# Optimization experiments

Measured on AMD Instinct MI355X. Metric: run time of the kernel, lower is better.

The kernel has to match this reference:

```python
import jax, jax.numpy as jnp
import numpy as np

NUM_EDGE_TYPES = 4
TIME_STEPS = (1, 1)  # one propagation step per layer, 2 layers
HIDDEN = 128
N_NODES = 50000
N_EDGES = 400000


def setup_inputs() -> dict:
    key = jax.random.key(0)
    ks = jax.random.split(key, 8)
    states = jax.random.normal(ks[0], (N_NODES, HIDDEN), jnp.float32)
    etype = jax.random.randint(ks[1], (N_EDGES,), 0, NUM_EDGE_TYPES, jnp.int32)
    src = jax.random.randint(ks[2], (N_EDGES,), 0, N_NODES, jnp.int32)
    dst = jax.random.randint(ks[3], (N_EDGES,), 0, N_NODES, jnp.int32)
    edges = jnp.stack([etype, src, dst], axis=-1)  # [E, 3] = (type, src, dst)
    L = len(TIME_STEPS)
    std = HIDDEN ** -0.5  # matches tf.random_normal_initializer(stddev=H**-0.5)
    type_W = jax.random.normal(ks[4], (L, NUM_EDGE_TYPES, HIDDEN, HIDDEN), jnp.float32) * std
    type_b = jax.random.normal(ks[5], (L, NUM_EDGE_TYPES, HIDDEN), jnp.float32) * std
    gru_kernel = jax.random.normal(ks[6], (L, HIDDEN, 3 * HIDDEN), jnp.float32) * std
    gru_rkernel = jax.random.normal(ks[7], (L, HIDDEN, 3 * HIDDEN), jnp.float32) * std
    gru_bias = jnp.zeros((L, 2, 3 * HIDDEN), jnp.float32)  # [input_bias, recurrent_bias]
    return dict(states=states, edges=edges, type_W=type_W, type_b=type_b,
                gru_kernel=gru_kernel, gru_rkernel=gru_rkernel, gru_bias=gru_bias)


def _gru_cell(x, h, kernel, rkernel, bias):
    # tf.keras.layers.GRUCell with defaults (reset_after=True, sigmoid/tanh)
    mx = x @ kernel + bias[0]   # [N, 3H]
    mh = h @ rkernel + bias[1]  # [N, 3H]
    xz, xr, xh = jnp.split(mx, 3, axis=-1)
    hz, hr, hh = jnp.split(mh, 3, axis=-1)
    z = jax.nn.sigmoid(xz + hz)
    r = jax.nn.sigmoid(xr + hr)
    c = jnp.tanh(xh + r * hh)
    return z * h + (1.0 - z) * c


def _propagate(h, layer_no, edges, type_W, type_b):
    etype, src, dst = edges[:, 0], edges[:, 1], edges[:, 2]
    src_states = h[src]  # [E, H] irregular gather
    msgs = jnp.zeros_like(src_states)
    # per-edge-type dense transform, combined via masking (jit-friendly
    # equivalent of tf.dynamic_partition + per-type matmul)
    for t in range(NUM_EDGE_TYPES):
        mt = src_states @ type_W[layer_no, t] + type_b[layer_no, t]
        msgs = msgs + jnp.where((etype == t)[:, None], mt, 0.0)
    # scatter-add messages into destination nodes
    return jax.ops.segment_sum(msgs, dst, num_segments=h.shape[0])


def reference(states, edges, type_W, type_b, gru_kernel, gru_rkernel, gru_bias):
    h = states
    for layer_no, steps in enumerate(TIME_STEPS):
        for _ in range(steps):
            agg = _propagate(h, layer_no, edges, type_W, type_b)
            h = _gru_cell(agg, h, gru_kernel[layer_no], gru_rkernel[layer_no], gru_bias[layer_no])
    return h
```

## Files before the change

### kernel.cpp

```cpp
#include <hip/hip_runtime.h>
#include <hip/hip_bf16.h>

#define H 128
#define NT 4
#define CAP4 40

typedef __attribute__((ext_vector_type(8))) _Float16 half8;
typedef __attribute__((ext_vector_type(8))) unsigned short ushort8;
typedef __attribute__((ext_vector_type(4))) float f32x4;

#if defined(__has_builtin)
#if __has_builtin(__builtin_amdgcn_global_load_lds)
#define HAS_GLL 1
#endif
#endif
#ifndef HAS_GLL
#define HAS_GLL 0
#endif

__device__ __forceinline__ float bf2f(unsigned short u) {
    union { unsigned int i; float f; } v;
    v.i = ((unsigned int)u) << 16;
    return v.f;
}

__device__ __forceinline__ unsigned short f2bf(float f) {
    union { float f; unsigned int i; } v;
    v.f = f;
    unsigned int x = v.i;
    unsigned int r = (x + 0x7fffu + ((x >> 16) & 1u)) >> 16;
    return (unsigned short)r;
}

__device__ __forceinline__ float fsigmoid(float x) {
    return 1.0f / (1.0f + __expf(-x));
}
__device__ __forceinline__ float ftanh(float x) {
    return 1.0f - 2.0f / (__expf(2.0f * x) + 1.0f);
}

__device__ __forceinline__ float readf(const void* p, long i, int isbf) {
    return isbf ? bf2f(((const unsigned short*)p)[i]) : ((const float*)p)[i];
}

__device__ __forceinline__ void gll16(const _Float16* g, _Float16* l) {
#if HAS_GLL
    __builtin_amdgcn_global_load_lds(
        (const __attribute__((address_space(1))) unsigned int*)g,
        (__attribute__((address_space(3))) unsigned int*)l, 16, 0, 0);
#else
    const int lane = threadIdx.x & 63;
    *(half8*)&l[lane * 8] = *(const half8*)g;
#endif
}

__device__ __forceinline__ half8 frag(const _Float16* lds, int r, int g) {
    return *(const half8*)&lds[r * 64 + ((g ^ (r & 7)) * 8)];
}

__global__ void detect_dtype(const unsigned short* __restrict__ states_u16,
                             int* __restrict__ flag) {
    __shared__ int cnt;
    if (threadIdx.x == 0) cnt = 0;
    __syncthreads();
    int local = 0;
    for (int i = threadIdx.x; i < 1024; i += 256) {
        unsigned short u = states_u16[2 * i];
        int e = (u >> 7) & 0xFF;
        if (e >= 96 && e <= 158) local++;
    }
    atomicAdd(&cnt, local);
    __syncthreads();
    if (threadIdx.x == 0) *flag = (cnt >= 512) ? 1 : 0;
}

__global__ void prep_all(
    const void* __restrict__ states, const void* __restrict__ type_W,
    const void* __restrict__ type_b, const void* __restrict__ gk,
    const void* __restrict__ gr, const void* __restrict__ grub,
    _Float16* __restrict__ h16, _Float16* __restrict__ BTw,
    _Float16* __restrict__ BTg, float* __restrict__ btab,
    float* __restrict__ gbsum, float* __restrict__ gb0c,
    float* __restrict__ gb1c, int* __restrict__ counts4,
    const int* __restrict__ flag,
    long NNH, int nBTw, int nBTg, int NC4, int LAYERS) {
    long i = (long)blockIdx.x * 256 + threadIdx.x;
    const int fl = *flag;
    if (i < NNH) {
        h16[i] = (_Float16)readf(states, i, fl);
        return;
    }
    i -= NNH;
    if (i < nBTw) {
        int l = (int)(i >> 16);
        int r16 = (int)(i & 65535);
        int cblk = r16 >> 13;
        int rem = r16 & 8191;
        int g = rem >> 7;
        int mm = (rem >> 3) & 15;
        int j = rem & 7;
        int c = cblk * 16 + mm;
        int k = g * 8 + j;
        int t = k >> 7, kk = k & 127;
        BTw[i] = (_Float16)readf(type_W, (((long)(l * NT + t) * H) + kk) * H + c, fl);
        return;
    }
    i -= nBTw;
    if (i < nBTg) {
        int l = (int)(i >> 17);
        int r17 = (int)(i & 131071);
        int ncblk = r17 >> 12;
        int rem = r17 & 4095;
        int g = rem >> 7;
        int mm = (rem >> 3) & 15;
        int j = rem & 7;
        int nc = ncblk * 16 + mm;
        int k = g * 8 + j;
        int gblk = nc >> 6, gate = (nc >> 4) & 3;
        int c = gblk * 16 + (nc & 15);
        float v = 0.0f;
        if (gate == 0) {
            v = (k < 128) ? readf(gk, ((long)l * H + k) * 384 + c, fl)
                          : readf(gr, ((long)l * H + (k - 128)) * 384 + c, fl);
        } else if (gate == 1) {
            v = (k < 128) ? readf(gk, ((long)l * H + k) * 384 + 128 + c, fl)
                          : readf(gr, ((long)l * H + (k - 128)) * 384 + 128 + c, fl);
        } else if (gate == 2) {
            if (k < 128) v = readf(gk, ((long)l * H + k) * 384 + 256 + c, fl);
        } else {
            if (k >= 128) v = readf(gr, ((long)l * H + (k - 128)) * 384 + 256 + c, fl);
        }
        BTg[i] = (_Float16)v;
        return;
    }
    i -= nBTg;
    if (i < NC4) {
        counts4[i] = 0;
        return;
    }
    i -= NC4;
    {
        int j = (int)i;
        if (j < LAYERS * NT * H) btab[j] = readf(type_b, j, fl);
        if (j < LAYERS * 256) {
            int l = j >> 8, c = j & 255;
            gbsum[j] = readf(grub, (long)l * 768 + c, fl) +
                       readf(grub, (long)l * 768 + 384 + c, fl);
        }
        if (j < LAYERS * H) {
            int l = j >> 7, c = j & 127;
            gb0c[j] = readf(grub, (long)l * 768 + 256 + c, fl);
            gb1c[j] = readf(grub, (long)l * 768 + 384 + 256 + c, fl);
        }
    }
}

__global__ void place_edges4(const int* __restrict__ edges, int* __restrict__ counts4,
                             int* __restrict__ buckets4, int NE) {
    int e = blockIdx.x * 256 + threadIdx.x;
    if (e >= NE) return;
    int t = edges[3 * e], src = edges[3 * e + 1], dst = edges[3 * e + 2];
    int slot = atomicAdd(&counts4[dst * 4 + t], 1);
    if (slot < CAP4) buckets4[((size_t)dst * 4 + t) * CAP4 + slot] = src;
}

__global__ __launch_bounds__(256) void gather4(
    const _Float16* __restrict__ h16, const int* __restrict__ counts4,
    const int* __restrict__ buckets4, _Float16* __restrict__ A4, int NN) {
    int wid = blockIdx.x * 4 + (threadIdx.x >> 6);
    int node = wid >> 2, q = wid & 3;
    int lane = threadIdx.x & 63;
    int e4 = lane >> 4, i = lane & 15;
    if (node >= NN) return;
    int cnt = counts4[node * 4 + q];
    if (cnt > CAP4) cnt = CAP4;
    const int* bkt = buckets4 + ((size_t)node * 4 + q) * CAP4;

    float acc[8] = {};
    for (int e = e4; e < cnt; e += 4) {
        int s = bkt[e];
        half8 v = *(const half8*)&h16[(size_t)s * H + i * 8];
#pragma unroll
        for (int j = 0; j < 8; j++) acc[j] += (float)v[j];
    }

#pragma unroll
    for (int j = 0; j < 8; j++) {
        acc[j] += __shfl_xor(acc[j], 16, 64);
        acc[j] += __shfl_xor(acc[j], 32, 64);
    }

    if (e4 == 0) {
        half8 o;
#pragma unroll
        for (int j = 0; j < 8; j++) o[j] = (_Float16)acc[j];
        *(half8*)&A4[((size_t)node * 4 + q) * H + i * 8] = o;
    }
}

__global__ __launch_bounds__(256, 4) void layer_fused(
    const _Float16* __restrict__ A4,
    const _Float16* __restrict__ h16,
    const _Float16* __restrict__ BTw,
    const _Float16* __restrict__ BTg,
    const float* __restrict__ btab,
    const int4* __restrict__ cnt4,
    const float* __restrict__ gbsum,
    const float* __restrict__ gb0c,
    const float* __restrict__ gb1c,
    _Float16* __restrict__ hnext,
    void* __restrict__ outbuf,
    const int* __restrict__ flag, int NN) {
    __shared__ __align__(16) _Float16 As[2048];
    __shared__ __align__(16) _Float16 Bs[8192];
    __shared__ __align__(16) _Float16 aggL[4096];
    __shared__ __align__(16) _Float16 hL[4096];

    const int row0 = blockIdx.x * 32;
    const int tid = threadIdx.x;
    const int wave = tid >> 6, lane = tid & 63;
    const int m = lane & 15, quad = lane >> 4;

    f32x4 acc[2][2] = {};
    for (int kc = 0; kc < 8; kc++) {
        __syncthreads();
        {
            int R = wave * 8;
            int rl = R + (lane >> 3);
            int rg = row0 + rl;
            if (rg >= NN) rg = NN - 1;
            int chunk = (lane & 7) ^ (rl & 7);
            gll16(A4 + (size_t)rg * 512 + kc * 64 + chunk * 8, As + R * 64);
        }
#pragma unroll
        for (int r = 0; r < 4; r++) {
            int u = r * 256 + tid;
            int cblk = u >> 7, gp = (u >> 4) & 7, mm = u & 15;
            gll16(BTw + cblk * 8192 + (kc * 8 + gp) * 128 + mm * 8,
                  Bs + (r * 256 + wave * 64) * 8);
        }
        __syncthreads();
#pragma unroll
        for (int ks = 0; ks < 2; ks++) {
            half8 a[2], b[2];
#pragma unroll
            for (int mt = 0; mt < 2; mt++)
                a[mt] = frag(As, mt * 16 + m, ks * 4 + quad);
#pragma unroll
            for (int nt = 0; nt < 2; nt++)
                b[nt] = *(const half8*)&Bs[(wave * 2 + nt) * 1024 +
                                           (ks * 4 + quad) * 128 + m * 8];
#pragma unroll
            for (int mt = 0; mt < 2; mt++)
#pragma unroll
                for (int nt = 0; nt < 2; nt++)
                    acc[mt][nt] = __builtin_amdgcn_mfma_f32_16x16x32_f16(
                        a[mt], b[nt], acc[mt][nt], 0, 0, 0);
        }
    }

    {
        int R = wave * 8;
        int rl = R + (lane >> 3);
        int rg = row0 + rl;
        if (rg >= NN) rg = NN - 1;
        int chunk = (lane & 7) ^ (rl & 7);
        gll16(h16 + (size_t)rg * H + chunk * 8, hL + R * 64);
        gll16(h16 + (size_t)rg * H + 64 + chunk * 8, hL + 2048 + R * 64);
    }

#pragma unroll
    for (int mt = 0; mt < 2; mt++) {
#pragma unroll
        for (int i = 0; i < 4; i++) {
            int rl = mt * 16 + quad * 4 + i;
            int rg = row0 + rl;
            if (rg >= NN) rg = NN - 1;
            int4 c4 = cnt4[rg];
#pragma unroll
            for (int nt = 0; nt < 2; nt++) {
                int c = wave * 32 + nt * 16 + m;
                float bias = c4.x * btab[c] + c4.y * btab[128 + c] +
                             c4.z * btab[256 + c] + c4.w * btab[384 + c];
                int sub = c >> 6, cc = c & 63, g = cc >> 3;
                aggL[sub * 2048 + rl * 64 + ((g ^ (rl & 7)) * 8) + (cc & 7)] =
                    (_Float16)(acc[mt][nt][i] + bias);
            }
        }
    }
    __syncthreads();

    _Float16* hout16 = Bs;
    const int fl = outbuf ? *flag : 0;
    const int y = wave;
#pragma unroll
    for (int ch = 0; ch < 2; ch++) {
        f32x4 p[2][4] = {};
        const int ncb0 = y * 8 + ch * 4;
#pragma unroll
        for (int kc = 0; kc < 4; kc++) {
            const int ntA = (kc < 2) ? 2 : 3;
            const _Float16* Asrc = (kc < 2) ? (aggL + kc * 2048)
                                            : (hL + (kc - 2) * 2048);
#pragma unroll
            for (int ks = 0; ks < 2; ks++) {
                const int gk = kc * 8 + ks * 4 + quad;
                half8 a0 = frag(Asrc, m, ks * 4 + quad);
                half8 a1 = frag(Asrc, 16 + m, ks * 4 + quad);
                half8 b0 = *(const half8*)&BTg[(size_t)(ncb0 + 0) * 4096 +
                                               gk * 128 + m * 8];
                half8 b1 = *(const half8*)&BTg[(size_t)(ncb0 + 1) * 4096 +
                                               gk * 128 + m * 8];
                half8 b2 = *(const half8*)&BTg[(size_t)(ncb0 + ntA) * 4096 +
                                               gk * 128 + m * 8];
                p[0][0] = __builtin_amdgcn_mfma_f32_16x16x32_f16(a0, b0, p[0][0], 0, 0, 0);
                p[1][0] = __builtin_amdgcn_mfma_f32_16x16x32_f16(a1, b0, p[1][0], 0, 0, 0);
                p[0][1] = __builtin_amdgcn_mfma_f32_16x16x32_f16(a0, b1, p[0][1], 0, 0, 0);
                p[1][1] = __builtin_amdgcn_mfma_f32_16x16x32_f16(a1, b1, p[1][1], 0, 0, 0);
                p[0][ntA] = __builtin_amdgcn_mfma_f32_16x16x32_f16(a0, b2, p[0][ntA], 0, 0, 0);
                p[1][ntA] = __builtin_amdgcn_mfma_f32_16x16x32_f16(a1, b2, p[1][ntA], 0, 0, 0);
            }
        }

        const int c = (2 * y + ch) * 16 + m;
        const float bz = gbsum[c];
        const float br = gbsum[128 + c];
        const float bx = gb0c[c];
        const float bh = gb1c[c];
        const int sub = c >> 6, cc = c & 63, hg = cc >> 3, hj = cc & 7;
#pragma unroll
        for (int mt = 0; mt < 2; mt++) {
#pragma unroll
            for (int i = 0; i < 4; i++) {
                int rl = mt * 16 + quad * 4 + i;
                int row = row0 + rl;
                float z = fsigmoid(p[mt][0][i] + bz);
                float r = fsigmoid(p[mt][1][i] + br);
                float ccand =
                    ftanh((p[mt][2][i] + bx) + r * (p[mt][3][i] + bh));
                float hv = (float)hL[sub * 2048 + rl * 64 +
                                     ((hg ^ (rl & 7)) * 8) + hj];
                float hn = z * hv + (1.0f - z) * ccand;
                if (outbuf) {
                    if (row < NN) {
                        size_t oi = (size_t)row * H + c;
                        if (fl) ((unsigned short*)outbuf)[oi] = f2bf(hn);
                        else    ((float*)outbuf)[oi] = hn;
                    }
                } else {
                    hout16[rl * 136 + c] = (_Float16)hn;
                }
            }
        }
    }

    if (!outbuf) {
        __syncthreads();
        int r = tid >> 3, s = tid & 7;
        int row = row0 + r;
        if (row < NN) {
            half8 v0 = *(const half8*)&hout16[r * 136 + s * 16];
            half8 v1 = *(const half8*)&hout16[r * 136 + s * 16 + 8];
            size_t o = (size_t)row * H + s * 16;
            *(half8*)&hnext[o] = v0;
            *(half8*)&hnext[o + 8] = v1;
        }
    }
}

extern "C" void kernel_launch(void* const* d_in, const int* in_sizes, int n_in,
                              void* d_out, int out_size, void* d_ws, size_t ws_size,
                              hipStream_t stream) {
    const void* states = d_in[0];
    const int*  edges  = (const int*)d_in[1];
    const void* type_W = d_in[2];
    const void* type_b = d_in[3];
    const void* gruk   = d_in[4];
    const void* grur   = d_in[5];
    const void* grub   = d_in[6];

    const int NN = in_sizes[0] / H;
    const int NE = in_sizes[1] / 3;
    const int nW = in_sizes[2];
    const int LAYERS = nW / (NT * H * H);

    char* w = (char*)d_ws;
    int* flag = (int*)w;                               w += 64;
    _Float16* h16A  = (_Float16*)w;                    w += (size_t)NN * H * 2;
    _Float16* h16B  = (_Float16*)w;                    w += (size_t)NN * H * 2;
    _Float16* A4    = (_Float16*)w;                    w += (size_t)NN * 4 * H * 2;
    _Float16* BTw = (_Float16*)w;                      w += (size_t)LAYERS * H * 512 * 2;
    _Float16* BTg = (_Float16*)w;                      w += (size_t)LAYERS * 512 * 256 * 2;
    float* btab  = (float*)w;                          w += (size_t)LAYERS * NT * H * 4;
    float* gbsum = (float*)w;                          w += (size_t)LAYERS * 256 * 4;
    float* gb0c  = (float*)w;                          w += (size_t)LAYERS * H * 4;
    float* gb1c  = (float*)w;                          w += (size_t)LAYERS * H * 4;
    int* counts4 = (int*)w;                            w += (size_t)NN * 4 * 4;
    int* buckets4 = (int*)w;

    detect_dtype<<<1, 256, 0, stream>>>((const unsigned short*)states, flag);

    const long NNH = (long)NN * H;
    const int nBTw = LAYERS * 65536;
    const int nBTg = LAYERS * 131072;
    const int NC4 = NN * 4;
    const long ptotal = NNH + nBTw + nBTg + NC4 + LAYERS * NT * H;
    prep_all<<<(int)((ptotal + 255) / 256), 256, 0, stream>>>(
        states, type_W, type_b, gruk, grur, grub,
        h16A, BTw, BTg, btab, gbsum, gb0c, gb1c, counts4, flag,
        NNH, nBTw, nBTg, NC4, LAYERS);

    place_edges4<<<(NE + 255) / 256, 256, 0, stream>>>(edges, counts4, buckets4, NE);

    const int rt32 = (NN + 31) / 32;
    const int nwt = NN;
    for (int L = 0; L < LAYERS; L++) {
        const _Float16* hcur = (L & 1) ? h16B : h16A;
        _Float16* hnext      = (L & 1) ? h16A : h16B;

        gather4<<<nwt, 256, 0, stream>>>(hcur, counts4, buckets4, A4, NN);

        layer_fused<<<rt32, 256, 0, stream>>>(
            A4, hcur,
            BTw + (size_t)L * H * 512,
            BTg + (size_t)L * 512 * 256,
            btab + (size_t)L * NT * H, (const int4*)counts4,
            gbsum + (size_t)L * 256, gb0c + (size_t)L * H, gb1c + (size_t)L * H,
            hnext, (L == LAYERS - 1) ? d_out : nullptr, flag, NN);
    }
}
```

Baseline: 292.8 us.

## Fold dtype detection into prep and remap gather to one wave per node

The separate dtype-detection kernel is removed. Each prep_all block now samples the states itself and derives the flag locally, which drops one launch and the global flag read, at the cost of redundant sampling work in every block. gather4 now assigns one wavefront per node, with each 16-lane group handling one edge type. The first eight bucket indices are loaded as vector int4s and the gathers are unrolled, replacing the old scheme of one wave per (node, type) with a cross-lane shuffle reduction. This cuts the gather grid by four and removes the shuffles and idle lanes, but each lane now walks its edges serially, so fewer loads are in flight per lane.

```diff
diff --git a/kernel.cpp b/kernel.cpp
--- a/kernel.cpp
+++ b/kernel.cpp
@@ -58,22 +58,6 @@
     return *(const half8*)&lds[r * 64 + ((g ^ (r & 7)) * 8)];
 }
 
-__global__ void detect_dtype(const unsigned short* __restrict__ states_u16,
-                             int* __restrict__ flag) {
-    __shared__ int cnt;
-    if (threadIdx.x == 0) cnt = 0;
-    __syncthreads();
-    int local = 0;
-    for (int i = threadIdx.x; i < 1024; i += 256) {
-        unsigned short u = states_u16[2 * i];
-        int e = (u >> 7) & 0xFF;
-        if (e >= 96 && e <= 158) local++;
-    }
-    atomicAdd(&cnt, local);
-    __syncthreads();
-    if (threadIdx.x == 0) *flag = (cnt >= 512) ? 1 : 0;
-}
-
 __global__ void prep_all(
     const void* __restrict__ states, const void* __restrict__ type_W,
     const void* __restrict__ type_b, const void* __restrict__ gk,
@@ -82,10 +66,26 @@
     _Float16* __restrict__ BTg, float* __restrict__ btab,
     float* __restrict__ gbsum, float* __restrict__ gb0c,
     float* __restrict__ gb1c, int* __restrict__ counts4,
-    const int* __restrict__ flag,
+    int* __restrict__ flag_out,
     long NNH, int nBTw, int nBTg, int NC4, int LAYERS) {
+    __shared__ int scnt;
+    if (threadIdx.x == 0) scnt = 0;
+    __syncthreads();
+    {
+        const unsigned short* su = (const unsigned short*)states;
+        int local = 0;
+        for (int t = threadIdx.x; t < 1024; t += 256) {
+            unsigned short u = su[2 * t];
+            int e = (u >> 7) & 0xFF;
+            if (e >= 96 && e <= 158) local++;
+        }
+        atomicAdd(&scnt, local);
+    }
+    __syncthreads();
+    const int fl = (scnt >= 512) ? 1 : 0;
+    if (blockIdx.x == 0 && threadIdx.x == 0) *flag_out = fl;
+
     long i = (long)blockIdx.x * 256 + threadIdx.x;
-    const int fl = *flag;
     if (i < NNH) {
         h16[i] = (_Float16)readf(states, i, fl);
         return;
@@ -167,35 +167,46 @@
 __global__ __launch_bounds__(256) void gather4(
     const _Float16* __restrict__ h16, const int* __restrict__ counts4,
     const int* __restrict__ buckets4, _Float16* __restrict__ A4, int NN) {
-    int wid = blockIdx.x * 4 + (threadIdx.x >> 6);
-    int node = wid >> 2, q = wid & 3;
+    int node = blockIdx.x * 4 + (threadIdx.x >> 6);
     int lane = threadIdx.x & 63;
-    int e4 = lane >> 4, i = lane & 15;
+    int q = lane >> 4, i = lane & 15;
     if (node >= NN) return;
+    const int* bkt = buckets4 + ((size_t)node * 4 + q) * CAP4;
+
+    int4 b0 = *(const int4*)bkt;
+    int4 b1 = *(const int4*)(bkt + 4);
     int cnt = counts4[node * 4 + q];
     if (cnt > CAP4) cnt = CAP4;
-    const int* bkt = buckets4 + ((size_t)node * 4 + q) * CAP4;
 
     float acc[8] = {};
-    for (int e = e4; e < cnt; e += 4) {
-        int s = bkt[e];
-        half8 v = *(const half8*)&h16[(size_t)s * H + i * 8];
-#pragma unroll
-        for (int j = 0; j < 8; j++) acc[j] += (float)v[j];
-    }
-
-#pragma unroll
-    for (int j = 0; j < 8; j++) {
-        acc[j] += __shfl_xor(acc[j], 16, 64);
-        acc[j] += __shfl_xor(acc[j], 32, 64);
-    }
-
-    if (e4 == 0) {
-        half8 o;
-#pragma unroll
-        for (int j = 0; j < 8; j++) o[j] = (_Float16)acc[j];
-        *(half8*)&A4[((size_t)node * 4 + q) * H + i * 8] = o;
-    }
+    {
+        int ss[8] = {b0.x, b0.y, b0.z, b0.w, b1.x, b1.y, b1.z, b1.w};
+#pragma unroll
+        for (int e = 0; e < 8; e++) {
+            if (e < cnt) {
+                half8 v = *(const half8*)&h16[(size_t)ss[e] * H + i * 8];
+#pragma unroll
+                for (int j = 0; j < 8; j++) acc[j] += (float)v[j];
+            }
+        }
+    }
+    for (int e = 8; e < cnt; e += 4) {
+        int4 bb = *(const int4*)(bkt + e);
+        int sr[4] = {bb.x, bb.y, bb.z, bb.w};
+#pragma unroll
+        for (int k = 0; k < 4; k++) {
+            if (e + k < cnt) {
+                half8 v = *(const half8*)&h16[(size_t)sr[k] * H + i * 8];
+#pragma unroll
+                for (int j = 0; j < 8; j++) acc[j] += (float)v[j];
+            }
+        }
+    }
+
+    half8 o;
+#pragma unroll
+    for (int j = 0; j < 8; j++) o[j] = (_Float16)acc[j];
+    *(half8*)&A4[((size_t)node * 4 + q) * H + i * 8] = o;
 }
 
 __global__ __launch_bounds__(256, 4) void layer_fused(
@@ -398,8 +409,6 @@
     int* counts4 = (int*)w;                            w += (size_t)NN * 4 * 4;
     int* buckets4 = (int*)w;
 
-    detect_dtype<<<1, 256, 0, stream>>>((const unsigned short*)states, flag);
-
     const long NNH = (long)NN * H;
     const int nBTw = LAYERS * 65536;
     const int nBTg = LAYERS * 131072;
@@ -413,12 +422,11 @@
     place_edges4<<<(NE + 255) / 256, 256, 0, stream>>>(edges, counts4, buckets4, NE);
 
     const int rt32 = (NN + 31) / 32;
-    const int nwt = NN;
     for (int L = 0; L < LAYERS; L++) {
         const _Float16* hcur = (L & 1) ? h16B : h16A;
         _Float16* hnext      = (L & 1) ? h16A : h16B;
 
-        gather4<<<nwt, 256, 0, stream>>>(hcur, counts4, buckets4, A4, NN);
+        gather4<<<(NN + 3) / 4, 256, 0, stream>>>(hcur, counts4, buckets4, A4, NN);
 
         layer_fused<<<rt32, 256, 0, stream>>>(
             A4, hcur,
```

Measured after the change: 312.1 us. 1.07x slower.
